# Optimization experiments

Measured on AMD Instinct MI355X. Metric: run time of the kernel, lower is better.

## Reference

```python
import jax, jax.numpy as jnp
import numpy as np

WS = (2, 7, 7)   # window size (d, h, w)
NH = 4           # num heads
EPS = 1e-5       # LayerNorm eps (torch default)


def _rel_index():
    wd, wh, ww = WS
    coords = np.stack(np.meshgrid(np.arange(wd), np.arange(wh), np.arange(ww), indexing='ij'))  # (3,wd,wh,ww)
    cf = coords.reshape(3, -1)                      # (3, N)
    rel = cf[:, :, None] - cf[:, None, :]           # (3, N, N)
    rel = rel.transpose(1, 2, 0).astype(np.int64)   # (N, N, 3)
    rel[..., 0] += wd - 1
    rel[..., 1] += wh - 1
    rel[..., 2] += ww - 1
    rel[..., 0] *= (2 * wh - 1) * (2 * ww - 1)
    rel[..., 1] *= (2 * ww - 1)
    return jnp.asarray(rel.sum(-1), dtype=jnp.int32)  # (N, N)


def setup_inputs() -> dict:
    key = jax.random.key(0)
    ks = jax.random.split(key, 6)
    C, CH = 128, 512
    TBL = (2 * WS[0] - 1) * (2 * WS[1] - 1) * (2 * WS[2] - 1)  # 507
    rn = lambda k, s, sc=0.02: jax.random.normal(k, s, jnp.float32) * sc
    return {
        'x': jax.random.normal(ks[0], (2, 8, 56, 56, C), jnp.float32),
        'norm1_w': jnp.ones((C,), jnp.float32), 'norm1_b': jnp.zeros((C,), jnp.float32),
        'qkv_w': rn(ks[1], (3 * C, C)), 'qkv_b': jnp.zeros((3 * C,), jnp.float32),
        'bias_table': rn(ks[2], (TBL, NH)),
        'proj_w': rn(ks[3], (C, C)), 'proj_b': jnp.zeros((C,), jnp.float32),
        'norm2_w': jnp.ones((C,), jnp.float32), 'norm2_b': jnp.zeros((C,), jnp.float32),
        'fc1_w': rn(ks[4], (CH, C)), 'fc1_b': jnp.zeros((CH,), jnp.float32),
        'fc2_w': rn(ks[5], (C, CH)), 'fc2_b': jnp.zeros((C,), jnp.float32),
        'rel_index': _rel_index(),
    }


def _layernorm(x, w, b):
    m = jnp.mean(x, axis=-1, keepdims=True)
    v = jnp.mean(jnp.square(x - m), axis=-1, keepdims=True)
    return (x - m) * jax.lax.rsqrt(v + EPS) * w + b


def reference(x, norm1_w, norm1_b, qkv_w, qkv_b, bias_table, proj_w, proj_b,
              norm2_w, norm2_b, fc1_w, fc1_b, fc2_w, fc2_b, rel_index):
    B, D, H, W, C = x.shape
    wd, wh, ww = WS
    N = wd * wh * ww
    hd = C // NH

    shortcut = x
    xn = _layernorm(x, norm1_w, norm1_b)
    # window partition: (B,D,H,W,C) -> (B*nW, N, C)
    xw = xn.reshape(B, D // wd, wd, H // wh, wh, W // ww, ww, C)
    xw = xw.transpose(0, 1, 3, 5, 2, 4, 6, 7).reshape(-1, N, C)
    B_ = xw.shape[0]

    qkv = (xw @ qkv_w.T + qkv_b).reshape(B_, N, 3, NH, hd).transpose(2, 0, 3, 1, 4)
    q, k, v = qkv[0] * (hd ** -0.5), qkv[1], qkv[2]   # (B_, NH, N, hd)
    attn = jnp.einsum('bhnd,bhmd->bhnm', q, k)
    bias = bias_table[rel_index.reshape(-1)].reshape(N, N, NH).transpose(2, 0, 1)  # (NH,N,N)
    attn = jax.nn.softmax(attn + bias[None], axis=-1)
    out = jnp.einsum('bhnm,bhmd->bhnd', attn, v).transpose(0, 2, 1, 3).reshape(B_, N, C)
    out = out @ proj_w.T + proj_b

    # window reverse: (B*nW, N, C) -> (B,D,H,W,C)
    xr = out.reshape(B, D // wd, H // wh, W // ww, wd, wh, ww, C)
    xr = xr.transpose(0, 1, 4, 2, 5, 3, 6, 7).reshape(B, D, H, W, C)

    x = shortcut + xr
    h = _layernorm(x, norm2_w, norm2_b)
    h = jax.nn.gelu(h @ fc1_w.T + fc1_b, approximate=False)  # torch nn.GELU = exact erf
    return x + (h @ fc2_w.T + fc2_b)
```

## Files before the change

### kernel.cpp

```cpp
#include <hip/hip_runtime.h>
#include <hip/hip_bf16.h>

typedef __hip_bfloat16 bf16;
typedef unsigned short u16t;
typedef unsigned int u32t;
typedef __attribute__((ext_vector_type(8))) short bf16x8_t;
typedef __attribute__((ext_vector_type(4))) float f32x4_t;

#define DEVI static __device__ __forceinline__

DEVI float u2f(u32t bits) { union { u32t u; float f; } v; v.u = bits; return v.f; }
DEVI float bflo(u32t u) { return u2f((u & 0xffffu) << 16); }
DEVI float bfhi(u32t u) { return u2f(u & 0xffff0000u); }
DEVI float sh2f(short s) { return u2f(((u32t)(u16t)s) << 16); }
DEVI float bf2f(bf16 h) { return __bfloat162float(h); }
DEVI bf16 f2bf(float f) { return __float2bfloat16(f); }
DEVI u16t f2bfbits(float f) {
  bf16 h = __float2bfloat16(f);
  union { bf16 h; u16t u; } v; v.h = h; return v.u;
}

DEVI void gl_lds16(const void* g, void* l) {
  __builtin_amdgcn_global_load_lds(
      (const __attribute__((address_space(1))) unsigned int*)g,
      (__attribute__((address_space(3))) unsigned int*)l, 16, 0, 0);
}

#define TOK   50176
#define NWIN  512
#define NTOK  98
#define NHEAD 4
#define HDIM  32
#define QSCALE 0.17677669529663687f

__global__ __launch_bounds__(256) void setup_k(
    const float* __restrict__ a, const float* __restrict__ b,
    const float* __restrict__ c, const float* __restrict__ d,
    bf16* __restrict__ o,
    const float* __restrict__ btab, const int* __restrict__ relidx,
    const float* __restrict__ qkv_b, float* __restrict__ BmatT,
    float* __restrict__ bsc) {
  int bx = blockIdx.x;
  if (bx < 768) {
    int i = bx * 256 + threadIdx.x;
    const float* s; int off;
    if (i < 49152)       { s = a; off = 0; }
    else if (i < 65536)  { s = b; off = 49152; }
    else if (i < 131072) { s = c; off = 65536; }
    else                 { s = d; off = 131072; }
    float v = s[i - off];
    if (i < 16384) v *= QSCALE;
    o[i] = f2bf(v);
  } else {
    int idx = (bx - 768) * 256 + threadIdx.x;
    if (idx < NTOK * NTOK) {
      int i = idx / NTOK, j = idx - i * NTOK;
      int r = relidx[idx] * NHEAD;
#pragma unroll
      for (int h = 0; h < NHEAD; h++)
        BmatT[(size_t)(h * NTOK + j) * 112 + i] = btab[r + h];
    }
    if (bx == 768 && threadIdx.x < 384)
      bsc[threadIdx.x] = qkv_b[threadIdx.x] * (threadIdx.x < 128 ? QSCALE : 1.0f);
  }
}

__global__ __launch_bounds__(256) void ln1_k(
    const float* __restrict__ x, const float* __restrict__ w,
    const float* __restrict__ b, bf16* __restrict__ o)
{
  const int wave = threadIdx.x >> 6, lane = threadIdx.x & 63;
  const int t = blockIdx.x * 4 + wave;
  const int c = lane << 1;
  float2 xv = *(const float2*)(x + (size_t)t * 128 + c);
  float x0 = xv.x, x1 = xv.y;
  float s = x0 + x1, ss = x0 * x0 + x1 * x1;
#pragma unroll
  for (int m = 32; m; m >>= 1) { s += __shfl_xor(s, m); ss += __shfl_xor(ss, m); }
  float mean = s * 0.0078125f;
  float var = ss * 0.0078125f - mean * mean;
  float rstd = rsqrtf(var + 1e-5f);
  float y0 = (x0 - mean) * rstd * w[c]     + b[c];
  float y1 = (x1 - mean) * rstd * w[c + 1] + b[c + 1];
  int wi = t % 56; int r = t / 56;
  int hi_ = r % 56; r /= 56;
  int di = r & 7; int bi = r >> 3;
  int nw = ((bi * 4 + (di >> 1)) * 8 + hi_ / 7) * 8 + wi / 7;
  int n  = ((di & 1) * 7 + hi_ % 7) * 7 + wi % 7;
  u32t ov = ((u32t)f2bfbits(y1) << 16) | (u32t)f2bfbits(y0);
  *(u32t*)((u16t*)o + (size_t)(nw * NTOK + n) * 128 + c) = ov;
}

DEVI int winrev(int grow) {
  int nw = grow / NTOK, n = grow - nw * NTOK;
  int wq = nw & 7, hq = (nw >> 3) & 7, dq = (nw >> 6) & 3, bb = nw >> 8;
  int wr = n % 7; int q7 = n / 7; int hr = q7 % 7, dr = q7 / 7;
  return ((bb * 8 + dq * 2 + dr) * 56 + hq * 7 + hr) * 56 + wq * 7 + wr;
}

template <int MODE, int NT16, int KT>
__global__ __launch_bounds__(256) void gemm3_k(
    const bf16* __restrict__ A, const bf16* __restrict__ W,
    const float* __restrict__ bias, const float* __restrict__ resX,
    const bf16* __restrict__ resB2, bf16* __restrict__ outB,
    bf16* __restrict__ outB2, float* __restrict__ outF,
    const float* __restrict__ lnw, const float* __restrict__ lnb, int N)
{
  __shared__ __align__(16) short As[128 * 128];
  __shared__ __align__(16) short Bs[NT16 * 16 * 128];
  const int K = KT * 128;
  const int tid = threadIdx.x;
  const int rowBase = blockIdx.y << 7;
  const int colBase = blockIdx.x * (NT16 * 16);
  const int wv = tid >> 6, lane = tid & 63;
  const int q = lane >> 4, r16 = lane & 15;
  const int mB = wv << 5;

  f32x4_t acc[2][NT16];
#pragma unroll
  for (int i = 0; i < 2; i++)
#pragma unroll
    for (int j = 0; j < NT16; j++) acc[i][j] = (f32x4_t){0.f, 0.f, 0.f, 0.f};

#pragma unroll
  for (int kt = 0; kt < KT; kt++) {
    const int kc = kt << 7;
#pragma unroll
    for (int t = 0; t < 8; t++) {
      int f = tid + (t << 8);
      int row = f >> 4, cs = (f & 15) ^ (row & 15);
      gl_lds16((const u16t*)A + (size_t)(rowBase + row) * K + kc + (cs << 3),
               &As[f << 3]);
    }
#pragma unroll
    for (int t = 0; t < NT16; t++) {
      int f = tid + (t << 8);
      int row = f >> 4, cs = (f & 15) ^ (row & 15);
      gl_lds16((const u16t*)W + (size_t)(colBase + row) * K + kc + (cs << 3),
               &Bs[f << 3]);
    }
    __syncthreads();
#pragma unroll
    for (int ks = 0; ks < 4; ks++) {
      bf16x8_t af[2], bfr[NT16];
#pragma unroll
      for (int mt = 0; mt < 2; mt++) {
        int row = mB + (mt << 4) + r16;
        int slot = ((ks << 2) + q) ^ (row & 15);
        af[mt] = *(const bf16x8_t*)&As[(row << 7) + (slot << 3)];
      }
#pragma unroll
      for (int nt = 0; nt < NT16; nt++) {
        int row = (nt << 4) + r16;
        int slot = ((ks << 2) + q) ^ (row & 15);
        bfr[nt] = *(const bf16x8_t*)&Bs[(row << 7) + (slot << 3)];
      }
#pragma unroll
      for (int mt = 0; mt < 2; mt++)
#pragma unroll
        for (int nt = 0; nt < NT16; nt++)
          acc[mt][nt] = __builtin_amdgcn_mfma_f32_16x16x32_bf16(
              af[mt], bfr[nt], acc[mt][nt], 0, 0, 0);
    }
    __syncthreads();
  }

  float bv[NT16];
#pragma unroll
  for (int nt = 0; nt < NT16; nt++) bv[nt] = bias[colBase + (nt << 4) + r16];

  if (MODE == 1) {
#pragma unroll
    for (int mt = 0; mt < 2; mt++)
#pragma unroll
      for (int reg = 0; reg < 4; reg++) {
        int lrow = mB + (mt << 4) + (q << 2) + reg;
#pragma unroll
        for (int nt = 0; nt < NT16; nt++)
          As[(lrow << 7) + (nt << 4) + r16] = (short)f2bfbits(acc[mt][nt][reg] + bv[nt]);
      }
    __syncthreads();
#pragma unroll
    for (int t = 0; t < 8; t++) {
      int f = tid + (t << 8);
      int row = f >> 4, c8 = (f & 15) << 3;
      int tt = winrev(rowBase + row);
      size_t ob = (size_t)tt * 128 + c8;
      float4 r0 = *(const float4*)(resX + ob);
      float4 r1 = *(const float4*)(resX + ob + 4);
      short* cs = &As[(row << 7) + c8];
      u16t pk[8];
      pk[0] = f2bfbits(sh2f(cs[0]) + r0.x); pk[1] = f2bfbits(sh2f(cs[1]) + r0.y);
      pk[2] = f2bfbits(sh2f(cs[2]) + r0.z); pk[3] = f2bfbits(sh2f(cs[3]) + r0.w);
      pk[4] = f2bfbits(sh2f(cs[4]) + r1.x); pk[5] = f2bfbits(sh2f(cs[5]) + r1.y);
      pk[6] = f2bfbits(sh2f(cs[6]) + r1.z); pk[7] = f2bfbits(sh2f(cs[7]) + r1.w);
      *(uint4*)((u16t*)outB + ob) = *(const uint4*)pk;
      *(uint4*)cs = *(const uint4*)pk;
    }
    __syncthreads();
    const int c = lane << 1;
    float2 lw = *(const float2*)(lnw + c);
    float2 lb = *(const float2*)(lnb + c);
#pragma unroll 4
    for (int rr = 0; rr < 32; rr++) {
      int row = (wv << 5) + rr;
      u32t u = *(const u32t*)&As[(row << 7) + c];
      float x0 = bflo(u), x1 = bfhi(u);
      float s = x0 + x1, ss = x0 * x0 + x1 * x1;
#pragma unroll
      for (int m = 32; m; m >>= 1) { s += __shfl_xor(s, m); ss += __shfl_xor(ss, m); }
      float mean = s * 0.0078125f;
      float var = ss * 0.0078125f - mean * mean;
      float rstd = rsqrtf(var + 1e-5f);
      float y0 = (x0 - mean) * rstd * lw.x + lb.x;
      float y1 = (x1 - mean) * rstd * lw.y + lb.y;
      int tt = winrev(rowBase + row);
      u32t ov = ((u32t)f2bfbits(y1) << 16) | (u32t)f2bfbits(y0);
      *(u32t*)((u16t*)outB2 + (size_t)tt * 128 + c) = ov;
    }
    return;
  }

  {
    constexpr int CW = NT16 * 16;
    constexpr int CPR = CW >> 3;
    constexpr int NIT = (128 * CPR) >> 8;
#pragma unroll
    for (int mt = 0; mt < 2; mt++)
#pragma unroll
      for (int reg = 0; reg < 4; reg++) {
        int lrow = mB + (mt << 4) + (q << 2) + reg;
#pragma unroll
        for (int nt = 0; nt < NT16; nt++) {
          float v = acc[mt][nt][reg] + bv[nt];
          As[lrow * CW + (nt << 4) + r16] = (short)f2bfbits(v);
        }
      }
    __syncthreads();
#pragma unroll
    for (int t = 0; t < NIT; t++) {
      int f = tid + (t << 8);
      int row = f / CPR, c8 = (f % CPR) << 3;
      size_t ob = (size_t)(rowBase + row) * N + colBase + c8;
      *(uint4*)((u16t*)outB + ob) = *(const uint4*)&As[row * CW + c8];
    }
  }
}

__global__ __launch_bounds__(256, 2) void mlp_fused_k(
    const bf16* __restrict__ Axn, const bf16* __restrict__ F1,
    const bf16* __restrict__ F2, const float* __restrict__ b1,
    const float* __restrict__ b2, const bf16* __restrict__ resB,
    float* __restrict__ out)
{
  __shared__ __align__(16) char smem[81920];
  short* As  = (short*)smem;
  short* F1s = (short*)(smem + 32768);
  short* F2s = (short*)(smem + 49152);
  short* Hs  = (short*)(smem + 65536);
  float* Cf  = (float*)smem;

  const int tid = threadIdx.x;
  const int rowBase = blockIdx.x << 7;
  const int wv = tid >> 6, lane = tid & 63;
  const int q = lane >> 4, r16 = lane & 15;
  const int mB = wv << 5;

#pragma unroll
  for (int t = 0; t < 8; t++) {
    int f = tid + (t << 8);
    int row = f >> 4, cs = (f & 15) ^ (row & 15);
    gl_lds16((const u16t*)Axn + (size_t)(rowBase + row) * 128 + (cs << 3),
             &As[f << 3]);
  }
#pragma unroll
  for (int t = 0; t < 4; t++) {
    int f = tid + (t << 8);
    int row = f >> 4, cs = (f & 15) ^ (row & 15);
    gl_lds16((const u16t*)F1 + (size_t)row * 128 + (cs << 3), &F1s[f << 3]);
  }
#pragma unroll
  for (int t = 0; t < 4; t++) {
    int f = tid + (t << 8);
    int row = f >> 3, cs = (f & 7) ^ (row & 7);
    gl_lds16((const u16t*)F2 + (size_t)row * 512 + (cs << 3), &F2s[f << 3]);
  }
  __syncthreads();

  f32x4_t oacc[2][8];
#pragma unroll
  for (int i = 0; i < 2; i++)
#pragma unroll
    for (int j = 0; j < 8; j++) oacc[i][j] = (f32x4_t){0.f, 0.f, 0.f, 0.f};

#pragma unroll 1
  for (int c = 0; c < 8; c++) {
    if (c > 0) {
#pragma unroll
      for (int t = 0; t < 4; t++) {
        int f = tid + (t << 8);
        int row = f >> 4, cs = (f & 15) ^ (row & 15);
        gl_lds16((const u16t*)F1 + (size_t)(c * 64 + row) * 128 + (cs << 3),
                 &F1s[f << 3]);
      }
#pragma unroll
      for (int t = 0; t < 4; t++) {
        int f = tid + (t << 8);
        int row = f >> 3, cs = (f & 7) ^ (row & 7);
        gl_lds16((const u16t*)F2 + (size_t)row * 512 + c * 64 + (cs << 3),
                 &F2s[f << 3]);
      }
      __syncthreads();
    }

    f32x4_t hacc[2][4];
#pragma unroll
    for (int i = 0; i < 2; i++)
#pragma unroll
      for (int j = 0; j < 4; j++) hacc[i][j] = (f32x4_t){0.f, 0.f, 0.f, 0.f};
#pragma unroll
    for (int ks = 0; ks < 4; ks++) {
      bf16x8_t af[2], bfr[4];
#pragma unroll
      for (int mt = 0; mt < 2; mt++) {
        int row = mB + (mt << 4) + r16;
        int slot = ((ks << 2) + q) ^ (row & 15);
        af[mt] = *(const bf16x8_t*)&As[(row << 7) + (slot << 3)];
      }
#pragma unroll
      for (int nt = 0; nt < 4; nt++) {
        int row = (nt << 4) + r16;
        int slot = ((ks << 2) + q) ^ (row & 15);
        bfr[nt] = *(const bf16x8_t*)&F1s[(row << 7) + (slot << 3)];
      }
#pragma unroll
      for (int mt = 0; mt < 2; mt++)
#pragma unroll
        for (int nt = 0; nt < 4; nt++)
          hacc[mt][nt] = __builtin_amdgcn_mfma_f32_16x16x32_bf16(
              af[mt], bfr[nt], hacc[mt][nt], 0, 0, 0);
    }

    float bb[4];
#pragma unroll
    for (int nt = 0; nt < 4; nt++) bb[nt] = b1[c * 64 + (nt << 4) + r16];
#pragma unroll
    for (int mt = 0; mt < 2; mt++)
#pragma unroll
      for (int reg = 0; reg < 4; reg++) {
        int lrow = mB + (mt << 4) + (q << 2) + reg;
#pragma unroll
        for (int nt = 0; nt < 4; nt++) {
          float v = hacc[mt][nt][reg] + bb[nt];
          v = 0.5f * v * (1.0f + erff(v * 0.70710678118654752f));
          int col = (nt << 4) + r16;
          int sp = (col >> 3) ^ (lrow & 7);
          Hs[(lrow << 6) + (sp << 3) + (col & 7)] = (short)f2bfbits(v);
        }
      }
    __syncthreads();

#pragma unroll
    for (int ks = 0; ks < 2; ks++) {
      bf16x8_t af[2], bfr[8];
#pragma unroll
      for (int mt = 0; mt < 2; mt++) {
        int row = mB + (mt << 4) + r16;
        int slot = ((ks << 2) + q) ^ (row & 7);
        af[mt] = *(const bf16x8_t*)&Hs[(row << 6) + (slot << 3)];
      }
#pragma unroll
      for (int nt = 0; nt < 8; nt++) {
        int row = (nt << 4) + r16;
        int slot = ((ks << 2) + q) ^ (row & 7);
        bfr[nt] = *(const bf16x8_t*)&F2s[(row << 6) + (slot << 3)];
      }
#pragma unroll
      for (int mt = 0; mt < 2; mt++)
#pragma unroll
        for (int nt = 0; nt < 8; nt++)
          oacc[mt][nt] = __builtin_amdgcn_mfma_f32_16x16x32_bf16(
              af[mt], bfr[nt], oacc[mt][nt], 0, 0, 0);
    }
    __syncthreads();
  }

  float bv[8];
#pragma unroll
  for (int nt = 0; nt < 8; nt++) bv[nt] = b2[(nt << 4) + r16];
#pragma unroll
  for (int mt = 0; mt < 2; mt++)
#pragma unroll
    for (int reg = 0; reg < 4; reg++) {
      int lrow = mB + (mt << 4) + (q << 2) + reg;
#pragma unroll
      for (int nt = 0; nt < 8; nt++)
        Cf[lrow * 132 + (nt << 4) + r16] = oacc[mt][nt][reg] + bv[nt];
    }
  __syncthreads();
#pragma unroll
  for (int t = 0; t < 16; t++) {
    int f = tid + (t << 8);
    int row = f >> 5, c4 = (f & 31) << 2;
    size_t ob = (size_t)(rowBase + row) * 128 + c4;
    const u16t* rp = (const u16t*)resB + ob;
    const float* cp = &Cf[row * 132 + c4];
    float4 v;
    v.x = cp[0] + sh2f(rp[0]);
    v.y = cp[1] + sh2f(rp[1]);
    v.z = cp[2] + sh2f(rp[2]);
    v.w = cp[3] + sh2f(rp[3]);
    *(float4*)(out + ob) = v;
  }
}

#define PSTR 136
__global__ __launch_bounds__(256) void attn_mfma_k(
    const bf16* __restrict__ qkv, const float* __restrict__ BmatT,
    bf16* __restrict__ out)
{
  __shared__ short Vt[32 * PSTR];
  __shared__ short Ps[112 * PSTR];
  const int nw = blockIdx.x, h = blockIdx.y;
  const int tid = threadIdx.x;
  const int wv = tid >> 6, lane = tid & 63;
  const int q = lane >> 4, r16 = lane & 15;

  for (int idx = tid; idx < 32 * 38; idx += 256) {
    int d = idx / 38, j = 98 + idx % 38;
    Vt[d * PSTR + j] = 0;
  }
  for (int idx = tid; idx < 112 * 12; idx += 256) {
    int r = idx / 12, c = (idx % 12) << 1;
    *(u32t*)&Ps[r * PSTR + 112 + c] = 0;
  }
  for (int idx = tid; idx < NTOK * 16; idx += 256) {
    int j = idx >> 4, d2 = (idx & 15) << 1;
    u32t uv = *(const u32t*)((const u16t*)qkv +
                             (size_t)(nw * NTOK + j) * 384 + 256 + h * 32 + d2);
    Vt[d2 * PSTR + j] = (short)(uv & 0xffffu);
    Vt[(d2 + 1) * PSTR + j] = (short)(uv >> 16);
  }
  __syncthreads();

  const int mt0 = wv;
  const bool has2 = (wv + 4) < 7;
  const int mt1 = has2 ? wv + 4 : wv;

  int i0 = mt0 * 16 + r16; if (i0 > NTOK - 1) i0 = NTOK - 1;
  int i1 = mt1 * 16 + r16; if (i1 > NTOK - 1) i1 = NTOK - 1;
  bf16x8_t aq0 = *(const bf16x8_t*)((const u16t*)qkv +
      (size_t)(nw * NTOK + i0) * 384 + h * 32 + (q << 3));
  bf16x8_t aq1 = *(const bf16x8_t*)((const u16t*)qkv +
      (size_t)(nw * NTOK + i1) * 384 + h * 32 + (q << 3));

  f32x4_t sc[2][7];
#pragma unroll
  for (int nt = 0; nt < 7; nt++) {
    int j = (nt << 4) + r16; if (j > NTOK - 1) j = NTOK - 1;
    const float* bRow = &BmatT[(size_t)(h * NTOK + j) * 112];
    bf16x8_t bk = *(const bf16x8_t*)((const u16t*)qkv +
        (size_t)(nw * NTOK + j) * 384 + 128 + h * 32 + (q << 3));
    f32x4_t b0 = *(const f32x4_t*)&bRow[mt0 * 16 + (q << 2)];
    f32x4_t b1 = *(const f32x4_t*)&bRow[mt1 * 16 + (q << 2)];
    sc[0][nt] = __builtin_amdgcn_mfma_f32_16x16x32_bf16(aq0, bk, b0, 0, 0, 0);
    sc[1][nt] = __builtin_amdgcn_mfma_f32_16x16x32_bf16(aq1, bk, b1, 0, 0, 0);
  }

#pragma unroll
  for (int sel = 0; sel < 2; sel++) {
    if (sel == 1 && !has2) break;
    int mtile = sel ? mt1 : mt0;
    int ibase = mtile * 16 + (q << 2);
    float s[4][7];
#pragma unroll
    for (int nt = 0; nt < 7; nt++) {
      int j = (nt << 4) + r16;
#pragma unroll
      for (int reg = 0; reg < 4; reg++) {
        int i = ibase + reg;
        s[reg][nt] = (i < NTOK && j < NTOK) ? sc[sel][nt][reg] : -1.0e30f;
      }
    }
#pragma unroll
    for (int reg = 0; reg < 4; reg++) {
      float m = -3.0e38f;
#pragma unroll
      for (int nt = 0; nt < 7; nt++) m = fmaxf(m, s[reg][nt]);
#pragma unroll
      for (int d = 8; d; d >>= 1) m = fmaxf(m, __shfl_xor(m, d));
      float sum = 0.f;
#pragma unroll
      for (int nt = 0; nt < 7; nt++) { s[reg][nt] = __expf(s[reg][nt] - m); sum += s[reg][nt]; }
#pragma unroll
      for (int d = 8; d; d >>= 1) sum += __shfl_xor(sum, d);
      float inv = 1.f / sum;
#pragma unroll
      for (int nt = 0; nt < 7; nt++)
        Ps[(ibase + reg) * PSTR + (nt << 4) + r16] =
            (short)f2bfbits(s[reg][nt] * inv);
    }
    f32x4_t o0 = {0.f, 0.f, 0.f, 0.f}, o1 = {0.f, 0.f, 0.f, 0.f};
#pragma unroll
    for (int kt = 0; kt < 4; kt++) {
      bf16x8_t ap = *(const bf16x8_t*)&Ps[(mtile * 16 + r16) * PSTR + (kt << 5) + (q << 3)];
      bf16x8_t bv0 = *(const bf16x8_t*)&Vt[r16 * PSTR + (kt << 5) + (q << 3)];
      bf16x8_t bv1 = *(const bf16x8_t*)&Vt[(16 + r16) * PSTR + (kt << 5) + (q << 3)];
      o0 = __builtin_amdgcn_mfma_f32_16x16x32_bf16(ap, bv0, o0, 0, 0, 0);
      o1 = __builtin_amdgcn_mfma_f32_16x16x32_bf16(ap, bv1, o1, 0, 0, 0);
    }
#pragma unroll
    for (int reg = 0; reg < 4; reg++) {
      int i = mtile * 16 + (q << 2) + reg;
      if (i < NTOK) {
        size_t ob = (size_t)(nw * NTOK + i) * 128 + h * 32;
        out[ob + r16] = f2bf(o0[reg]);
        out[ob + 16 + r16] = f2bf(o1[reg]);
      }
    }
  }
}

extern "C" void kernel_launch(void* const* d_in, const int* in_sizes, int n_in,
                              void* d_out, int out_size, void* d_ws, size_t ws_size,
                              hipStream_t stream) {
  const float* x      = (const float*)d_in[0];
  const float* n1w    = (const float*)d_in[1];
  const float* n1b    = (const float*)d_in[2];
  const float* qkv_w  = (const float*)d_in[3];
  const float* qkv_b  = (const float*)d_in[4];
  const float* btab   = (const float*)d_in[5];
  const float* proj_w = (const float*)d_in[6];
  const float* proj_b = (const float*)d_in[7];
  const float* n2w    = (const float*)d_in[8];
  const float* n2b    = (const float*)d_in[9];
  const float* fc1_w  = (const float*)d_in[10];
  const float* fc1_b  = (const float*)d_in[11];
  const float* fc2_w  = (const float*)d_in[12];
  const float* fc2_b  = (const float*)d_in[13];
  const int*   relidx = (const int*)d_in[14];

  const size_t Asz = (size_t)TOK * 128 * 2;
  char* ws = (char*)d_ws;
  bf16* wbf   = (bf16*)ws;
  bf16* qkvw16  = wbf;
  bf16* projw16 = wbf + 49152;
  bf16* fc1w16  = wbf + 65536;
  bf16* fc2w16  = wbf + 131072;
  float* BmatT = (float*)(ws + 393216);
  float* bsc   = (float*)(ws + 393216 + 175616);
  char* R = ws + (1 << 20);
  bf16* xw    = (bf16*)d_out;
  bf16* attn  = (bf16*)d_out;
  bf16* qkv   = (bf16*)R;
  bf16* x2    = (bf16*)R;
  bf16* xn2   = (bf16*)(R + Asz);
  float* out  = (float*)d_out;

  setup_k<<<806, 256, 0, stream>>>(qkv_w, proj_w, fc1_w, fc2_w, wbf,
                                   btab, relidx, qkv_b, BmatT, bsc);
  ln1_k<<<TOK / 4, 256, 0, stream>>>(x, n1w, n1b, xw);
  gemm3_k<0, 8, 1><<<dim3(3, TOK / 128), 256, 0, stream>>>(
      xw, qkvw16, bsc, nullptr, nullptr, qkv, nullptr, nullptr,
      nullptr, nullptr, 384);
  attn_mfma_k<<<dim3(NWIN, NHEAD), 256, 0, stream>>>(qkv, BmatT, attn);
  gemm3_k<1, 8, 1><<<dim3(1, TOK / 128), 256, 0, stream>>>(
      attn, projw16, proj_b, x, nullptr, x2, xn2, nullptr, n2w, n2b, 128);
  mlp_fused_k<<<TOK / 128, 256, 0, stream>>>(
      xn2, fc1w16, fc2w16, fc1_b, fc2_b, x2, out);
}
```

Baseline: 212.8 us.

## Fuse LayerNorm1 and window partition into the QKV projection GEMM

After: 212.3 us. No clear change (-0.2%).

```diff
diff --git a/kernel.cpp b/kernel.cpp
--- a/kernel.cpp
+++ b/kernel.cpp
@@ -65,37 +65,109 @@
   }
 }
 
-__global__ __launch_bounds__(256) void ln1_k(
-    const float* __restrict__ x, const float* __restrict__ w,
-    const float* __restrict__ b, bf16* __restrict__ o)
-{
-  const int wave = threadIdx.x >> 6, lane = threadIdx.x & 63;
-  const int t = blockIdx.x * 4 + wave;
-  const int c = lane << 1;
-  float2 xv = *(const float2*)(x + (size_t)t * 128 + c);
-  float x0 = xv.x, x1 = xv.y;
-  float s = x0 + x1, ss = x0 * x0 + x1 * x1;
-#pragma unroll
-  for (int m = 32; m; m >>= 1) { s += __shfl_xor(s, m); ss += __shfl_xor(ss, m); }
-  float mean = s * 0.0078125f;
-  float var = ss * 0.0078125f - mean * mean;
-  float rstd = rsqrtf(var + 1e-5f);
-  float y0 = (x0 - mean) * rstd * w[c]     + b[c];
-  float y1 = (x1 - mean) * rstd * w[c + 1] + b[c + 1];
-  int wi = t % 56; int r = t / 56;
-  int hi_ = r % 56; r /= 56;
-  int di = r & 7; int bi = r >> 3;
-  int nw = ((bi * 4 + (di >> 1)) * 8 + hi_ / 7) * 8 + wi / 7;
-  int n  = ((di & 1) * 7 + hi_ % 7) * 7 + wi % 7;
-  u32t ov = ((u32t)f2bfbits(y1) << 16) | (u32t)f2bfbits(y0);
-  *(u32t*)((u16t*)o + (size_t)(nw * NTOK + n) * 128 + c) = ov;
-}
-
 DEVI int winrev(int grow) {
   int nw = grow / NTOK, n = grow - nw * NTOK;
   int wq = nw & 7, hq = (nw >> 3) & 7, dq = (nw >> 6) & 3, bb = nw >> 8;
   int wr = n % 7; int q7 = n / 7; int hr = q7 % 7, dr = q7 / 7;
   return ((bb * 8 + dq * 2 + dr) * 56 + hq * 7 + hr) * 56 + wq * 7 + wr;
+}
+
+__global__ __launch_bounds__(256) void qkvln_k(
+    const float* __restrict__ x, const float* __restrict__ n1w,
+    const float* __restrict__ n1b, const bf16* __restrict__ W,
+    const float* __restrict__ bsc, bf16* __restrict__ qkvO)
+{
+  __shared__ __align__(16) short As[64 * 128];
+  __shared__ __align__(16) short Bs[128 * 128];
+  const int tid = threadIdx.x;
+  const int rowBase = blockIdx.x << 6;
+  const int wv = tid >> 6, lane = tid & 63;
+  const int q = lane >> 4, r16 = lane & 15;
+
+#pragma unroll
+  for (int t = 0; t < 8; t++) {
+    int f = tid + (t << 8);
+    int row = f >> 4, cs = (f & 15) ^ (row & 15);
+    gl_lds16((const u16t*)W + (size_t)row * 128 + (cs << 3), &Bs[f << 3]);
+  }
+
+  {
+    const int c = lane << 1;
+    float lw0 = n1w[c], lw1 = n1w[c + 1];
+    float lb0 = n1b[c], lb1 = n1b[c + 1];
+#pragma unroll
+    for (int rr = 0; rr < 16; rr++) {
+      int row = (wv << 4) + rr;
+      int tt = winrev(rowBase + row);
+      float2 xv = *(const float2*)(x + (size_t)tt * 128 + c);
+      float x0 = xv.x, x1 = xv.y;
+      float s = x0 + x1, ss = x0 * x0 + x1 * x1;
+#pragma unroll
+      for (int m = 32; m; m >>= 1) { s += __shfl_xor(s, m); ss += __shfl_xor(ss, m); }
+      float mean = s * 0.0078125f;
+      float var = ss * 0.0078125f - mean * mean;
+      float rstd = rsqrtf(var + 1e-5f);
+      float y0 = (x0 - mean) * rstd * lw0 + lb0;
+      float y1 = (x1 - mean) * rstd * lw1 + lb1;
+      u32t ov = ((u32t)f2bfbits(y1) << 16) | (u32t)f2bfbits(y0);
+      int slot = (lane >> 2) ^ (row & 15);
+      *(u32t*)&As[(row << 7) + (slot << 3) + ((lane & 3) << 1)] = ov;
+    }
+  }
+  __syncthreads();
+
+#pragma unroll 1
+  for (int qt = 0; qt < 3; qt++) {
+    if (qt > 0) {
+#pragma unroll
+      for (int t = 0; t < 8; t++) {
+        int f = tid + (t << 8);
+        int row = f >> 4, cs = (f & 15) ^ (row & 15);
+        gl_lds16((const u16t*)W + (size_t)((qt << 7) + row) * 128 + (cs << 3),
+                 &Bs[f << 3]);
+      }
+      __syncthreads();
+    }
+    f32x4_t acc[8];
+#pragma unroll
+    for (int j = 0; j < 8; j++) acc[j] = (f32x4_t){0.f, 0.f, 0.f, 0.f};
+#pragma unroll
+    for (int ks = 0; ks < 4; ks++) {
+      int rowA = (wv << 4) + r16;
+      int slotA = ((ks << 2) + q) ^ (rowA & 15);
+      bf16x8_t af = *(const bf16x8_t*)&As[(rowA << 7) + (slotA << 3)];
+      bf16x8_t bfr[8];
+#pragma unroll
+      for (int nt = 0; nt < 8; nt++) {
+        int row = (nt << 4) + r16;
+        int slot = ((ks << 2) + q) ^ (row & 15);
+        bfr[nt] = *(const bf16x8_t*)&Bs[(row << 7) + (slot << 3)];
+      }
+#pragma unroll
+      for (int nt = 0; nt < 8; nt++)
+        acc[nt] = __builtin_amdgcn_mfma_f32_16x16x32_bf16(af, bfr[nt], acc[nt], 0, 0, 0);
+    }
+    float bv[8];
+#pragma unroll
+    for (int nt = 0; nt < 8; nt++) bv[nt] = bsc[(qt << 7) + (nt << 4) + r16];
+    __syncthreads();
+#pragma unroll
+    for (int reg = 0; reg < 4; reg++) {
+      int lrow = (wv << 4) + (q << 2) + reg;
+#pragma unroll
+      for (int nt = 0; nt < 8; nt++)
+        Bs[(lrow << 7) + (nt << 4) + r16] = (short)f2bfbits(acc[nt][reg] + bv[nt]);
+    }
+    __syncthreads();
+#pragma unroll
+    for (int t = 0; t < 4; t++) {
+      int f = tid + (t << 8);
+      int row = f >> 4, c8 = (f & 15) << 3;
+      size_t ob = (size_t)(rowBase + row) * 384 + (qt << 7) + c8;
+      *(uint4*)((u16t*)qkvO + ob) = *(const uint4*)&Bs[(row << 7) + c8];
+    }
+    if (qt < 2) __syncthreads();
+  }
 }
 
 template <int MODE, int NT16, int KT>
@@ -550,7 +622,6 @@
   float* BmatT = (float*)(ws + 393216);
   float* bsc   = (float*)(ws + 393216 + 175616);
   char* R = ws + (1 << 20);
-  bf16* xw    = (bf16*)d_out;
   bf16* attn  = (bf16*)d_out;
   bf16* qkv   = (bf16*)R;
   bf16* x2    = (bf16*)R;
@@ -559,10 +630,7 @@
 
   setup_k<<<806, 256, 0, stream>>>(qkv_w, proj_w, fc1_w, fc2_w, wbf,
                                    btab, relidx, qkv_b, BmatT, bsc);
-  ln1_k<<<TOK / 4, 256, 0, stream>>>(x, n1w, n1b, xw);
-  gemm3_k<0, 8, 1><<<dim3(3, TOK / 128), 256, 0, stream>>>(
-      xw, qkvw16, bsc, nullptr, nullptr, qkv, nullptr, nullptr,
-      nullptr, nullptr, 384);
+  qkvln_k<<<TOK / 64, 256, 0, stream>>>(x, n1w, n1b, qkvw16, bsc, qkv);
   attn_mfma_k<<<dim3(NWIN, NHEAD), 256, 0, stream>>>(qkv, BmatT, attn);
   gemm3_k<1, 8, 1><<<dim3(1, TOK / 128), 256, 0, stream>>>(
       attn, projw16, proj_b, x, nullptr, x2, xn2, nullptr, n2w, n2b, 128);
```
